# Performance work log

Measured on AMD Instinct MI355X. Metric: run time of the kernel, lower is better.

The kernel has to match this reference:

```python
import jax, jax.numpy as jnp
import numpy as np

N_NODES = 50000
N_POOLED = 25000
N_EDGES = 800000
D = 64
NUM_LAYERS = 4
LN_EPS = 1e-5
LEAKY_SLOPE = 0.01


def setup_inputs() -> dict:
    key = jax.random.key(0)
    k_x, k_e, k_i, k_w = jax.random.split(key, 4)
    x = jax.random.normal(k_x, (N_POOLED, D), dtype=jnp.float32)
    edge_index = jax.random.randint(k_e, (2, N_EDGES), 0, N_NODES, dtype=jnp.int64)
    # unique sorted indices of kept nodes (as produced by top-k pooling)
    perm = jax.random.permutation(k_i, N_NODES)
    idx = jnp.sort(perm[:N_POOLED]).astype(jnp.int64)
    Ws = jax.random.normal(k_w, (NUM_LAYERS, D, D), dtype=jnp.float32) / np.sqrt(D)
    bs = jnp.zeros((NUM_LAYERS, D), dtype=jnp.float32)
    gammas = jnp.ones((NUM_LAYERS, D), dtype=jnp.float32)
    betas = jnp.zeros((NUM_LAYERS, D), dtype=jnp.float32)
    return {"x": x, "edge_index": edge_index, "idx": idx,
            "Ws": Ws, "bs": bs, "gammas": gammas, "betas": betas}


def _layer_norm(x, gamma, beta):
    mu = jnp.mean(x, axis=-1, keepdims=True)
    xc = x - mu
    var = jnp.mean(xc * xc, axis=-1, keepdims=True)
    return xc * jax.lax.rsqrt(var + LN_EPS) * gamma + beta


def reference(x, edge_index, idx, Ws, bs, gammas, betas):
    # Unpool (layer 0): scatter pooled features into full-size zero tensor.
    cur = jnp.zeros((N_NODES, D), dtype=x.dtype).at[idx].set(x)

    # GCN normalization with self loops (shared across layers; graph is fixed).
    loop = jnp.arange(N_NODES, dtype=edge_index.dtype)
    src = jnp.concatenate([edge_index[0], loop])
    dst = jnp.concatenate([edge_index[1], loop])
    deg = jax.ops.segment_sum(jnp.ones_like(dst, dtype=x.dtype), dst,
                              num_segments=N_NODES)
    dinv = jax.lax.rsqrt(jnp.maximum(deg, 1.0))  # deg >= 1 (self loops)
    norm = (dinv[src] * dinv[dst])[:, None]      # [E+N, 1]

    h = None
    for l in range(NUM_LAYERS):
        # GCNConv: X W, then D^{-1/2}(A+I)D^{-1/2} aggregation, then bias.
        xw = cur @ Ws[l]
        agg = jax.ops.segment_sum(xw[src] * norm, dst, num_segments=N_NODES)
        agg = agg + bs[l]
        y = _layer_norm(agg, gammas[l], betas[l])
        act = jnp.where(y > 0, y, LEAKY_SLOPE * y)  # LeakyReLU(0.01)
        # dropout p=0.3 is identity in eval mode
        h = act * 0.5 if h is None else h + act * 0.5
        cur = act  # subsequent unpools are identity (sizes already match)
    return h
```

## Files before the change

### kernel.cpp

```cpp
#include <hip/hip_runtime.h>
#include <hip/hip_fp16.h>

#define NN 50000
#define NP 25000
#define NE 800000
#define DD 64
#define NL 4


__device__ __forceinline__ ushort f2bf(float f) {
    unsigned u = __float_as_uint(f);
    unsigned r = (u + 0x7fffu + ((u >> 16) & 1u)) >> 16;
    return (ushort)r;
}

__device__ __forceinline__ float4 bf4_to_f4(uint a, uint b) {
    float4 r;
    r.x = __uint_as_float(a << 16);
    r.y = __uint_as_float(a & 0xffff0000u);
    r.z = __uint_as_float(b << 16);
    r.w = __uint_as_float(b & 0xffff0000u);
    return r;
}

__device__ __forceinline__ float4 ld_bf16x4(const uint2* p) {
    uint2 q = *p;
    return bf4_to_f4(q.x, q.y);
}


__global__ void count_edges_k(const int* __restrict__ dst, int* __restrict__ cnt,
                              int* __restrict__ rank, int E) {
    int e = blockIdx.x * 256 + threadIdx.x;
    if (e < E) rank[e] = atomicAdd(&cnt[dst[e]], 1);
}

__global__ void scan_local_k(const int* __restrict__ cnt, int* __restrict__ rowptr,
                             int* __restrict__ bsum, int n) {
    __shared__ int tmp[1024];
    int t = threadIdx.x;
    int i = blockIdx.x * 1024 + t;
    int v = (i < n) ? cnt[i] : 0;
    tmp[t] = v;
    __syncthreads();
    for (int off = 1; off < 1024; off <<= 1) {
        int a = (t >= off) ? tmp[t - off] : 0;
        __syncthreads();
        tmp[t] += a;
        __syncthreads();
    }
    if (i < n) rowptr[i] = tmp[t] - v;
    if (t == 1023) bsum[blockIdx.x] = tmp[1023];
}

__global__ void scan_sums_k(int* bsum, int nb, int* rowptr, int n) {
    int t = threadIdx.x;
    int v = (t < nb) ? bsum[t] : 0;
    int s = v;
#pragma unroll
    for (int o = 1; o < 64; o <<= 1) {
        int u = __shfl_up(s, o);
        if (t >= o) s += u;
    }
    if (t < nb) bsum[t] = s - v;
    if (t == nb - 1) rowptr[n] = s;
}

__global__ void finalize_k(int* __restrict__ rowptr, const int* __restrict__ bsum,
                           const int* __restrict__ cnt, float* __restrict__ dinv, int n) {
    int i = blockIdx.x * 1024 + threadIdx.x;
    if (i < n) {
        rowptr[i] += bsum[blockIdx.x];
        dinv[i] = rsqrtf((float)(cnt[i] + 1));
    }
}

__global__ void fill_csr_k(const int* __restrict__ src, const int* __restrict__ dst,
                           const int* __restrict__ rank, const int* __restrict__ rowptr,
                           const float* __restrict__ dinv, uint* __restrict__ csr, int E) {
    int e = blockIdx.x * 256 + threadIdx.x;
    if (e >= E) return;
    int s = src[e], d = dst[e];
    int p = rowptr[d] + rank[e];
    float w = dinv[s] * dinv[d];
    uint h = (uint)__half_as_ushort(__float2half_rn(w));
    csr[p] = (uint)s | (h << 16);
}


__global__ void scatter_x_k(const float4* __restrict__ x4, const int* __restrict__ idx,
                            ushort4* __restrict__ c0) {
    int i = blockIdx.x * 256 + threadIdx.x;
    if (i >= NP * 16) return;
    int row = i >> 4, q = i & 15;
    float4 v = x4[i];
    ushort4 o;
    o.x = f2bf(v.x); o.y = f2bf(v.y); o.z = f2bf(v.z); o.w = f2bf(v.w);
    c0[(size_t)idx[row] * 16 + q] = o;
}


__global__ void gemm64_k(const uint2* __restrict__ in2, const float* __restrict__ W,
                         ushort* __restrict__ out) {
    __shared__ float sW[64][64];
    __shared__ float srow[16][64];
    int t = threadIdx.x;
    const float4* W4 = (const float4*)W;
    float4* sW4 = (float4*)sW;
#pragma unroll
    for (int j = 0; j < 4; ++j) sW4[t + 256 * j] = W4[t + 256 * j];
    int r0 = blockIdx.x * 16;
    float4 val = ld_bf16x4(in2 + (size_t)r0 * 16 + t);
    *(float4*)&srow[t >> 4][4 * (t & 15)] = val;
    __syncthreads();
    int r = t >> 4;
    int c4 = (t & 15) * 4;
    float ax = 0.f, ay = 0.f, az = 0.f, aw = 0.f;
#pragma unroll
    for (int k = 0; k < 64; ++k) {
        float a = srow[r][k];
        float4 w = *(const float4*)&sW[k][c4];
        ax += a * w.x; ay += a * w.y; az += a * w.z; aw += a * w.w;
    }
    ushort4 o;
    o.x = f2bf(ax); o.y = f2bf(ay); o.z = f2bf(az); o.w = f2bf(aw);
    *(ushort4*)&out[(size_t)(r0 + r) * 64 + c4] = o;
}


__global__ void agg_ln_k(const uint4* __restrict__ xw4, const int* __restrict__ rowptr,
                         const uint* __restrict__ csr, const float* __restrict__ dinv,
                         const float4* __restrict__ bias4, const float4* __restrict__ gamma4,
                         const float4* __restrict__ beta4, uint4* next,
                         const uint4* c1, const uint4* c2, const uint4* c3,
                         float4* outp, int last) {
    int tid = threadIdx.x;
    int l8 = tid & 7;
    int v = blockIdx.x * 32 + (tid >> 3);
    if (v >= NN) return;
    float dv = dinv[v];
    int jb = rowptr[v], je = rowptr[v + 1];
    float4 aLo, aHi;
    {
        uint4 q = xw4[(size_t)v * 8 + l8];
        float4 lo = bf4_to_f4(q.x, q.y), hi = bf4_to_f4(q.z, q.w);
        float s = dv * dv;
        aLo.x = s * lo.x; aLo.y = s * lo.y; aLo.z = s * lo.z; aLo.w = s * lo.w;
        aHi.x = s * hi.x; aHi.y = s * hi.y; aHi.z = s * hi.z; aHi.w = s * hi.w;
    }
#define UNPK(E) ((int)((E) & 0xffffu))
#define WGT(E)  __half2float(__ushort_as_half((ushort)((E) >> 16)))
    for (int j = jb; j < je; j += 8) {
        uint e0 = csr[j];
        uint e1 = csr[min(j + 1, je - 1)];
        uint e2 = csr[min(j + 2, je - 1)];
        uint e3 = csr[min(j + 3, je - 1)];
        uint e4 = csr[min(j + 4, je - 1)];
        uint e5 = csr[min(j + 5, je - 1)];
        uint e6 = csr[min(j + 6, je - 1)];
        uint e7 = csr[min(j + 7, je - 1)];
        float w0 = WGT(e0);
        float w1 = (j + 1 < je) ? WGT(e1) : 0.f;
        float w2 = (j + 2 < je) ? WGT(e2) : 0.f;
        float w3 = (j + 3 < je) ? WGT(e3) : 0.f;
        float w4 = (j + 4 < je) ? WGT(e4) : 0.f;
        float w5 = (j + 5 < je) ? WGT(e5) : 0.f;
        float w6 = (j + 6 < je) ? WGT(e6) : 0.f;
        float w7 = (j + 7 < je) ? WGT(e7) : 0.f;
        uint4 q0 = xw4[(size_t)UNPK(e0) * 8 + l8];
        uint4 q1 = xw4[(size_t)UNPK(e1) * 8 + l8];
        uint4 q2 = xw4[(size_t)UNPK(e2) * 8 + l8];
        uint4 q3 = xw4[(size_t)UNPK(e3) * 8 + l8];
        uint4 q4 = xw4[(size_t)UNPK(e4) * 8 + l8];
        uint4 q5 = xw4[(size_t)UNPK(e5) * 8 + l8];
        uint4 q6 = xw4[(size_t)UNPK(e6) * 8 + l8];
        uint4 q7 = xw4[(size_t)UNPK(e7) * 8 + l8];
#define ACC(Q, W) { \
        float4 lo = bf4_to_f4(Q.x, Q.y), hi = bf4_to_f4(Q.z, Q.w); \
        aLo.x += W * lo.x; aLo.y += W * lo.y; aLo.z += W * lo.z; aLo.w += W * lo.w; \
        aHi.x += W * hi.x; aHi.y += W * hi.y; aHi.z += W * hi.z; aHi.w += W * hi.w; }
        ACC(q0, w0) ACC(q1, w1) ACC(q2, w2) ACC(q3, w3)
        ACC(q4, w4) ACC(q5, w5) ACC(q6, w6) ACC(q7, w7)
#undef ACC
    }
#undef UNPK
#undef WGT
    float4 bLo = bias4[2 * l8], bBhi = bias4[2 * l8 + 1];
    aLo.x += bLo.x; aLo.y += bLo.y; aLo.z += bLo.z; aLo.w += bLo.w;
    aHi.x += bBhi.x; aHi.y += bBhi.y; aHi.z += bBhi.z; aHi.w += bBhi.w;
    float s = aLo.x + aLo.y + aLo.z + aLo.w + aHi.x + aHi.y + aHi.z + aHi.w;
#pragma unroll
    for (int o = 1; o <= 4; o <<= 1) s += __shfl_xor(s, o);
    float mu = s * (1.0f / 64.0f);
    float4 cLo = make_float4(aLo.x - mu, aLo.y - mu, aLo.z - mu, aLo.w - mu);
    float4 cHi = make_float4(aHi.x - mu, aHi.y - mu, aHi.z - mu, aHi.w - mu);
    float q2v = cLo.x * cLo.x + cLo.y * cLo.y + cLo.z * cLo.z + cLo.w * cLo.w
              + cHi.x * cHi.x + cHi.y * cHi.y + cHi.z * cHi.z + cHi.w * cHi.w;
#pragma unroll
    for (int o = 1; o <= 4; o <<= 1) q2v += __shfl_xor(q2v, o);
    float rs = rsqrtf(q2v * (1.0f / 64.0f) + 1e-5f);
    float4 gLo = gamma4[2 * l8], gHi = gamma4[2 * l8 + 1];
    float4 tLo = beta4[2 * l8],  tHi = beta4[2 * l8 + 1];
    float4 yLo = make_float4(cLo.x * rs * gLo.x + tLo.x, cLo.y * rs * gLo.y + tLo.y,
                             cLo.z * rs * gLo.z + tLo.z, cLo.w * rs * gLo.w + tLo.w);
    float4 yHi = make_float4(cHi.x * rs * gHi.x + tHi.x, cHi.y * rs * gHi.y + tHi.y,
                             cHi.z * rs * gHi.z + tHi.z, cHi.w * rs * gHi.w + tHi.w);
    float4 eLo = make_float4(yLo.x > 0.f ? yLo.x : 0.01f * yLo.x,
                             yLo.y > 0.f ? yLo.y : 0.01f * yLo.y,
                             yLo.z > 0.f ? yLo.z : 0.01f * yLo.z,
                             yLo.w > 0.f ? yLo.w : 0.01f * yLo.w);
    float4 eHi = make_float4(yHi.x > 0.f ? yHi.x : 0.01f * yHi.x,
                             yHi.y > 0.f ? yHi.y : 0.01f * yHi.y,
                             yHi.z > 0.f ? yHi.z : 0.01f * yHi.z,
                             yHi.w > 0.f ? yHi.w : 0.01f * yHi.w);
    if (!last) {
        uint4 o;
        o.x = (uint)f2bf(eLo.x) | ((uint)f2bf(eLo.y) << 16);
        o.y = (uint)f2bf(eLo.z) | ((uint)f2bf(eLo.w) << 16);
        o.z = (uint)f2bf(eHi.x) | ((uint)f2bf(eHi.y) << 16);
        o.w = (uint)f2bf(eHi.z) | ((uint)f2bf(eHi.w) << 16);
        next[(size_t)v * 8 + l8] = o;
    } else {
        uint4 u1 = c1[(size_t)v * 8 + l8];
        uint4 u2 = c2[(size_t)v * 8 + l8];
        uint4 u3 = c3[(size_t)v * 8 + l8];
        float4 p1 = bf4_to_f4(u1.x, u1.y), p1h = bf4_to_f4(u1.z, u1.w);
        float4 p2 = bf4_to_f4(u2.x, u2.y), p2h = bf4_to_f4(u2.z, u2.w);
        float4 p3 = bf4_to_f4(u3.x, u3.y), p3h = bf4_to_f4(u3.z, u3.w);
        float4 oLo, oHi;
        oLo.x = 0.5f * (p1.x + p2.x + p3.x + eLo.x);
        oLo.y = 0.5f * (p1.y + p2.y + p3.y + eLo.y);
        oLo.z = 0.5f * (p1.z + p2.z + p3.z + eLo.z);
        oLo.w = 0.5f * (p1.w + p2.w + p3.w + eLo.w);
        oHi.x = 0.5f * (p1h.x + p2h.x + p3h.x + eHi.x);
        oHi.y = 0.5f * (p1h.y + p2h.y + p3h.y + eHi.y);
        oHi.z = 0.5f * (p1h.z + p2h.z + p3h.z + eHi.z);
        oHi.w = 0.5f * (p1h.w + p2h.w + p3h.w + eHi.w);
        outp[(size_t)v * 16 + 2 * l8]     = oLo;
        outp[(size_t)v * 16 + 2 * l8 + 1] = oHi;
    }
}


extern "C" void kernel_launch(void* const* d_in, const int* in_sizes, int n_in,
                              void* d_out, int out_size, void* d_ws, size_t ws_size,
                              hipStream_t stream) {
    const float* x      = (const float*)d_in[0];
    const int*   ei     = (const int*)d_in[1];
    const int*   src    = ei;
    const int*   dst    = ei + NE;
    const int*   idx    = (const int*)d_in[2];
    const float* Ws     = (const float*)d_in[3];
    const float* bs     = (const float*)d_in[4];
    const float* gammas = (const float*)d_in[5];
    const float* betas  = (const float*)d_in[6];
    float* out = (float*)d_out;

    char* w = (char*)d_ws;
    auto alloc = [&](size_t bytes) -> char* {
        char* p = w;
        w += (bytes + 255) & ~(size_t)255;
        return p;
    };
    ushort* c[NL];
    for (int l = 0; l < NL; ++l) c[l] = (ushort*)alloc((size_t)NN * 64 * 2);
    ushort* xw    = (ushort*)alloc((size_t)NN * 64 * 2);
    int*   cnt    = (int*)alloc((size_t)NN * 4);
    int*   rowptr = (int*)alloc((size_t)(NN + 1) * 4);
    int*   rank   = (int*)alloc((size_t)NE * 4);
    float* dinv   = (float*)alloc((size_t)NN * 4);
    int*   bsum   = (int*)alloc(64 * 4);
    uint*  csr    = (uint*)alloc((size_t)NE * 4);

    hipMemsetAsync(cnt, 0, (size_t)NN * 4, stream);
    hipMemsetAsync(c[0], 0, (size_t)NN * 64 * 2, stream);

    count_edges_k<<<(NE + 255) / 256, 256, 0, stream>>>(dst, cnt, rank, NE);
    int nb = (NN + 1023) / 1024;
    scan_local_k<<<nb, 1024, 0, stream>>>(cnt, rowptr, bsum, NN);
    scan_sums_k<<<1, 64, 0, stream>>>(bsum, nb, rowptr, NN);
    finalize_k<<<nb, 1024, 0, stream>>>(rowptr, bsum, cnt, dinv, NN);
    fill_csr_k<<<(NE + 255) / 256, 256, 0, stream>>>(src, dst, rank, rowptr, dinv,
                                                     csr, NE);
    scatter_x_k<<<(NP * 16 + 255) / 256, 256, 0, stream>>>((const float4*)x, idx,
                                                           (ushort4*)c[0]);

    int agrid = (NN + 31) / 32;
    for (int l = 0; l < NL; ++l) {
        gemm64_k<<<NN / 16, 256, 0, stream>>>((const uint2*)c[l], Ws + (size_t)l * 64 * 64,
                                              xw);
        int last = (l == NL - 1);
        agg_ln_k<<<agrid, 256, 0, stream>>>((const uint4*)xw, rowptr, csr, dinv,
                                            (const float4*)(bs + l * 64),
                                            (const float4*)(gammas + l * 64),
                                            (const float4*)(betas + l * 64),
                                            last ? nullptr : (uint4*)c[l + 1],
                                            (const uint4*)c[1], (const uint4*)c[2],
                                            (const uint4*)c[3], (float4*)out, last);
    }
}
```

Baseline: 204.6 us.

## Pad CSR rows to multiples of eight and merge setup kernels

Each CSR row is padded to a multiple of 8 entries, with the padding zero-filled so it carries weight 0 and source 0. The aggregation loop can then load edge descriptors as aligned uint4 pairs, prefetched one iteration ahead, with no bounds clamps or per-edge weight masking. The three scan kernels are replaced by a single one-block scan that also computes dinv, and the CSR fill and x scatter are fused into one launch. This trades fewer launches and simpler inner-loop indexing for an extra memset of the enlarged CSR, wasted gathers on padded slots, and a serial single-block scan.

Result: slower. 321.4 us (+57.1%).

```diff
diff --git a/kernel.cpp b/kernel.cpp
--- a/kernel.cpp
+++ b/kernel.cpp
@@ -6,6 +6,7 @@
 #define NE 800000
 #define DD 64
 #define NL 4
+#define CSR_CAP (NE + 7 * NN + 16)
 
 
 __device__ __forceinline__ ushort f2bf(float f) {
@@ -35,68 +36,59 @@
     if (e < E) rank[e] = atomicAdd(&cnt[dst[e]], 1);
 }
 
-__global__ void scan_local_k(const int* __restrict__ cnt, int* __restrict__ rowptr,
-                             int* __restrict__ bsum, int n) {
-    __shared__ int tmp[1024];
+__global__ void scan_all_k(const int* __restrict__ cnt, int* __restrict__ rowptr,
+                           float* __restrict__ dinv, int n) {
+    __shared__ int tsum[1024];
     int t = threadIdx.x;
-    int i = blockIdx.x * 1024 + t;
-    int v = (i < n) ? cnt[i] : 0;
-    tmp[t] = v;
+    int base = t * 49;
+    int s = 0;
+    for (int k = 0; k < 49; ++k) {
+        int i = base + k;
+        if (i < n) s += (cnt[i] + 7) & ~7;
+    }
+    tsum[t] = s;
     __syncthreads();
     for (int off = 1; off < 1024; off <<= 1) {
-        int a = (t >= off) ? tmp[t - off] : 0;
+        int a = (t >= off) ? tsum[t - off] : 0;
         __syncthreads();
-        tmp[t] += a;
+        tsum[t] += a;
         __syncthreads();
     }
-    if (i < n) rowptr[i] = tmp[t] - v;
-    if (t == 1023) bsum[blockIdx.x] = tmp[1023];
-}
-
-__global__ void scan_sums_k(int* bsum, int nb, int* rowptr, int n) {
-    int t = threadIdx.x;
-    int v = (t < nb) ? bsum[t] : 0;
-    int s = v;
-#pragma unroll
-    for (int o = 1; o < 64; o <<= 1) {
-        int u = __shfl_up(s, o);
-        if (t >= o) s += u;
-    }
-    if (t < nb) bsum[t] = s - v;
-    if (t == nb - 1) rowptr[n] = s;
-}
-
-__global__ void finalize_k(int* __restrict__ rowptr, const int* __restrict__ bsum,
-                           const int* __restrict__ cnt, float* __restrict__ dinv, int n) {
-    int i = blockIdx.x * 1024 + threadIdx.x;
-    if (i < n) {
-        rowptr[i] += bsum[blockIdx.x];
-        dinv[i] = rsqrtf((float)(cnt[i] + 1));
-    }
-}
-
-__global__ void fill_csr_k(const int* __restrict__ src, const int* __restrict__ dst,
-                           const int* __restrict__ rank, const int* __restrict__ rowptr,
-                           const float* __restrict__ dinv, uint* __restrict__ csr, int E) {
-    int e = blockIdx.x * 256 + threadIdx.x;
-    if (e >= E) return;
-    int s = src[e], d = dst[e];
-    int p = rowptr[d] + rank[e];
-    float w = dinv[s] * dinv[d];
-    uint h = (uint)__half_as_ushort(__float2half_rn(w));
-    csr[p] = (uint)s | (h << 16);
-}
-
-
-__global__ void scatter_x_k(const float4* __restrict__ x4, const int* __restrict__ idx,
-                            ushort4* __restrict__ c0) {
-    int i = blockIdx.x * 256 + threadIdx.x;
-    if (i >= NP * 16) return;
-    int row = i >> 4, q = i & 15;
-    float4 v = x4[i];
-    ushort4 o;
-    o.x = f2bf(v.x); o.y = f2bf(v.y); o.z = f2bf(v.z); o.w = f2bf(v.w);
-    c0[(size_t)idx[row] * 16 + q] = o;
+    int run = tsum[t] - s;
+    for (int k = 0; k < 49; ++k) {
+        int i = base + k;
+        if (i < n) {
+            int c = cnt[i];
+            rowptr[i] = run;
+            run += (c + 7) & ~7;
+            dinv[i] = rsqrtf((float)(c + 1));
+        }
+    }
+    if (t == 1023) rowptr[n] = run;
+}
+
+__global__ void fill_scatter_k(const int* __restrict__ src, const int* __restrict__ dst,
+                               const int* __restrict__ rank, const int* __restrict__ rowptr,
+                               const float* __restrict__ dinv, uint* __restrict__ csr,
+                               const float4* __restrict__ x4, const int* __restrict__ idx,
+                               ushort4* __restrict__ c0) {
+    int b = blockIdx.x;
+    if (b < 3125) {
+        int e = b * 256 + threadIdx.x;
+        int s = src[e], d = dst[e];
+        int p = rowptr[d] + rank[e];
+        float w = dinv[s] * dinv[d];
+        uint h = (uint)__half_as_ushort(__float2half_rn(w));
+        csr[p] = (uint)s | (h << 16);
+    } else {
+        int i = (b - 3125) * 256 + threadIdx.x;
+        if (i >= NP * 16) return;
+        int row = i >> 4, q = i & 15;
+        float4 v = x4[i];
+        ushort4 o;
+        o.x = f2bf(v.x); o.y = f2bf(v.y); o.z = f2bf(v.z); o.w = f2bf(v.w);
+        c0[(size_t)idx[row] * 16 + q] = o;
+    }
 }
 
 
@@ -138,6 +130,7 @@
     int l8 = tid & 7;
     int v = blockIdx.x * 32 + (tid >> 3);
     if (v >= NN) return;
+    const uint4* csrq = (const uint4*)csr;
     float dv = dinv[v];
     int jb = rowptr[v], je = rowptr[v + 1];
     float4 aLo, aHi;
@@ -148,33 +141,22 @@
         aLo.x = s * lo.x; aLo.y = s * lo.y; aLo.z = s * lo.z; aLo.w = s * lo.w;
         aHi.x = s * hi.x; aHi.y = s * hi.y; aHi.z = s * hi.z; aHi.w = s * hi.w;
     }
-#define UNPK(E) ((int)((E) & 0xffffu))
+    uint4 ca = csrq[jb >> 2];
+    uint4 cb = csrq[(jb >> 2) + 1];
 #define WGT(E)  __half2float(__ushort_as_half((ushort)((E) >> 16)))
     for (int j = jb; j < je; j += 8) {
-        uint e0 = csr[j];
-        uint e1 = csr[min(j + 1, je - 1)];
-        uint e2 = csr[min(j + 2, je - 1)];
-        uint e3 = csr[min(j + 3, je - 1)];
-        uint e4 = csr[min(j + 4, je - 1)];
-        uint e5 = csr[min(j + 5, je - 1)];
-        uint e6 = csr[min(j + 6, je - 1)];
-        uint e7 = csr[min(j + 7, je - 1)];
-        float w0 = WGT(e0);
-        float w1 = (j + 1 < je) ? WGT(e1) : 0.f;
-        float w2 = (j + 2 < je) ? WGT(e2) : 0.f;
-        float w3 = (j + 3 < je) ? WGT(e3) : 0.f;
-        float w4 = (j + 4 < je) ? WGT(e4) : 0.f;
-        float w5 = (j + 5 < je) ? WGT(e5) : 0.f;
-        float w6 = (j + 6 < je) ? WGT(e6) : 0.f;
-        float w7 = (j + 7 < je) ? WGT(e7) : 0.f;
-        uint4 q0 = xw4[(size_t)UNPK(e0) * 8 + l8];
-        uint4 q1 = xw4[(size_t)UNPK(e1) * 8 + l8];
-        uint4 q2 = xw4[(size_t)UNPK(e2) * 8 + l8];
-        uint4 q3 = xw4[(size_t)UNPK(e3) * 8 + l8];
-        uint4 q4 = xw4[(size_t)UNPK(e4) * 8 + l8];
-        uint4 q5 = xw4[(size_t)UNPK(e5) * 8 + l8];
-        uint4 q6 = xw4[(size_t)UNPK(e6) * 8 + l8];
-        uint4 q7 = xw4[(size_t)UNPK(e7) * 8 + l8];
+        uint4 na = csrq[(j >> 2) + 2];
+        uint4 nb = csrq[(j >> 2) + 3];
+        uint4 q0 = xw4[(size_t)(ca.x & 0xffffu) * 8 + l8];
+        uint4 q1 = xw4[(size_t)(ca.y & 0xffffu) * 8 + l8];
+        uint4 q2 = xw4[(size_t)(ca.z & 0xffffu) * 8 + l8];
+        uint4 q3 = xw4[(size_t)(ca.w & 0xffffu) * 8 + l8];
+        uint4 q4 = xw4[(size_t)(cb.x & 0xffffu) * 8 + l8];
+        uint4 q5 = xw4[(size_t)(cb.y & 0xffffu) * 8 + l8];
+        uint4 q6 = xw4[(size_t)(cb.z & 0xffffu) * 8 + l8];
+        uint4 q7 = xw4[(size_t)(cb.w & 0xffffu) * 8 + l8];
+        float w0 = WGT(ca.x), w1 = WGT(ca.y), w2 = WGT(ca.z), w3 = WGT(ca.w);
+        float w4 = WGT(cb.x), w5 = WGT(cb.y), w6 = WGT(cb.z), w7 = WGT(cb.w);
 #define ACC(Q, W) { \
         float4 lo = bf4_to_f4(Q.x, Q.y), hi = bf4_to_f4(Q.z, Q.w); \
         aLo.x += W * lo.x; aLo.y += W * lo.y; aLo.z += W * lo.z; aLo.w += W * lo.w; \
@@ -182,8 +164,8 @@
         ACC(q0, w0) ACC(q1, w1) ACC(q2, w2) ACC(q3, w3)
         ACC(q4, w4) ACC(q5, w5) ACC(q6, w6) ACC(q7, w7)
 #undef ACC
-    }
-#undef UNPK
+        ca = na; cb = nb;
+    }
 #undef WGT
     float4 bLo = bias4[2 * l8], bBhi = bias4[2 * l8 + 1];
     aLo.x += bLo.x; aLo.y += bLo.y; aLo.z += bLo.z; aLo.w += bLo.w;
@@ -269,21 +251,16 @@
     int*   rowptr = (int*)alloc((size_t)(NN + 1) * 4);
     int*   rank   = (int*)alloc((size_t)NE * 4);
     float* dinv   = (float*)alloc((size_t)NN * 4);
-    int*   bsum   = (int*)alloc(64 * 4);
-    uint*  csr    = (uint*)alloc((size_t)NE * 4);
+    uint*  csr    = (uint*)alloc((size_t)CSR_CAP * 4);
 
     hipMemsetAsync(cnt, 0, (size_t)NN * 4, stream);
     hipMemsetAsync(c[0], 0, (size_t)NN * 64 * 2, stream);
+    hipMemsetAsync(csr, 0, (size_t)CSR_CAP * 4, stream);
 
     count_edges_k<<<(NE + 255) / 256, 256, 0, stream>>>(dst, cnt, rank, NE);
-    int nb = (NN + 1023) / 1024;
-    scan_local_k<<<nb, 1024, 0, stream>>>(cnt, rowptr, bsum, NN);
-    scan_sums_k<<<1, 64, 0, stream>>>(bsum, nb, rowptr, NN);
-    finalize_k<<<nb, 1024, 0, stream>>>(rowptr, bsum, cnt, dinv, NN);
-    fill_csr_k<<<(NE + 255) / 256, 256, 0, stream>>>(src, dst, rank, rowptr, dinv,
-                                                     csr, NE);
-    scatter_x_k<<<(NP * 16 + 255) / 256, 256, 0, stream>>>((const float4*)x, idx,
-                                                           (ushort4*)c[0]);
+    scan_all_k<<<1, 1024, 0, stream>>>(cnt, rowptr, dinv, NN);
+    fill_scatter_k<<<3125 + 1563, 256, 0, stream>>>(src, dst, rank, rowptr, dinv, csr,
+                                                    (const float4*)x, idx, (ushort4*)c[0]);
 
     int agrid = (NN + 31) / 32;
     for (int l = 0; l < NL; ++l) {
```
